# Kernel tuning notes

Measured on AMD Instinct MI355X. Metric: run time of the kernel, lower is better.

## Reference

```python
import jax, jax.numpy as jnp
import numpy as np

NUM_HEADS = 8
CH_PER_HEAD = 32
NUM_GROUPS = 32
EPS = 1e-5
SCALE = CH_PER_HEAD ** (-0.25)


def setup_inputs() -> dict:
    key = jax.random.key(0)
    ks = jax.random.split(key, 6)
    B, C, H, W = 2, 256, 64, 64
    hid = NUM_HEADS * CH_PER_HEAD  # 256
    s = 1.0 / np.sqrt(C)
    return {
        "x": jax.random.normal(ks[0], (B, C, H, W), dtype=jnp.float32),
        "gamma": jnp.ones((C,), jnp.float32),
        "beta": jnp.zeros((C,), jnp.float32),
        "wq": jax.random.normal(ks[1], (hid, C), jnp.float32) * s,
        "bq": jnp.zeros((hid,), jnp.float32),
        "wk": jax.random.normal(ks[2], (hid, C), jnp.float32) * s,
        "bk": jnp.zeros((hid,), jnp.float32),
        "wv": jax.random.normal(ks[3], (hid, C), jnp.float32) * s,
        "bv": jnp.zeros((hid,), jnp.float32),
        "wout": jax.random.normal(ks[4], (C, hid), jnp.float32) * s,
        "bout": jnp.zeros((C,), jnp.float32),
    }


def _group_norm(x, gamma, beta):
    b, c, h, w = x.shape
    xg = x.reshape(b, NUM_GROUPS, c // NUM_GROUPS, h, w)
    mu = jnp.mean(xg, axis=(2, 3, 4), keepdims=True)
    var = jnp.var(xg, axis=(2, 3, 4), keepdims=True)
    xg = (xg - mu) * jax.lax.rsqrt(var + EPS)
    return xg.reshape(b, c, h, w) * gamma[None, :, None, None] + beta[None, :, None, None]


def reference(x, gamma, beta, wq, bq, wk, bk, wv, bv, wout, bout):
    b, c, h, w = x.shape
    n = h * w
    x_n = _group_norm(x, gamma, beta).reshape(b, c, n)  # b c n (self-attention: embedding = x_n)
    # 1x1 convs == pointwise linear over the channel dim
    q = jnp.einsum('oc,bcn->bon', wq, x_n) + bq[None, :, None]
    k = jnp.einsum('oc,bcn->bon', wk, x_n) + bk[None, :, None]
    v = jnp.einsum('oc,bcn->bon', wv, x_n) + bv[None, :, None]
    # split heads: b (h d) n -> b h d n
    d = CH_PER_HEAD
    q = q.reshape(b, NUM_HEADS, d, n)
    k = k.reshape(b, NUM_HEADS, d, n)
    v = v.reshape(b, NUM_HEADS, d, n)
    attn = jax.nn.softmax(jnp.einsum('bhdi,bhdj->bhij', q * SCALE, k * SCALE), axis=-1)
    out = jnp.einsum('bhij,bhdj->bhdi', attn, v).reshape(b, NUM_HEADS * d, n)
    out = jnp.einsum('oc,bcn->bon', wout, out) + bout[None, :, None]
    out = out.reshape(b, -1, h, w)
    return x + out  # shapes match -> residual
```

## Files before the change

### kernel.cpp

```cpp
#include <hip/hip_runtime.h>
#include <hip/hip_bf16.h>
#include <stdint.h>

typedef unsigned short u16;
typedef float f32x4 __attribute__((ext_vector_type(4)));
typedef float f32x16 __attribute__((ext_vector_type(16)));
typedef short bf16x8 __attribute__((ext_vector_type(8)));

#define NSP 4096
#define CDIM 256
#define HID 256
#define NH 8
#define DH 32
#define NG 32
#define CPG 8
#define BATCH 2
#define SPLIT 4
#define GN_EPS 1e-5f
#define QK2_SCALE 0.25503488f

#define MFMA32(A, B, C) __builtin_amdgcn_mfma_f32_32x32x16_bf16(A, B, C, 0, 0, 0)
#define MFMA16(A, B, C) __builtin_amdgcn_mfma_f32_16x16x32_bf16(A, B, C, 0, 0, 0)

__device__ __forceinline__ float bf2f(u16 u) {
    union { uint32_t i; float f; } v; v.i = ((uint32_t)u) << 16; return v.f;
}
__device__ __forceinline__ u16 f2bf(float f) {
    union { float f; uint32_t i; } v; v.f = f;
    uint32_t b = v.i;
    return (u16)((b + 0x7FFFu + ((b >> 16) & 1u)) >> 16);
}

__device__ __forceinline__ void gload16(const u16* g, u16* lds) {
    __builtin_amdgcn_global_load_lds(
        (const __attribute__((address_space(1))) uint32_t*)g,
        (__attribute__((address_space(3))) uint32_t*)lds, 16, 0, 0);
}

__device__ __forceinline__ void pl32swap(uint32_t& a, uint32_t& b) {
    asm("v_permlane32_swap_b32 %0, %1" : "+v"(a), "+v"(b));
}

__global__ void gn_stats(const float* __restrict__ x, float* __restrict__ stats,
                         const float* __restrict__ wq, const float* __restrict__ wk,
                         const float* __restrict__ wv, const float* __restrict__ wout,
                         u16* __restrict__ wcat) {
    int blk = blockIdx.x;
#pragma unroll
    for (int i = 0; i < 16; i++) {
        int idx = blk * 4096 + i * 256 + threadIdx.x;
        const float* src = (idx < 65536) ? wq : (idx < 131072) ? wk : (idx < 196608) ? wv : wout;
        wcat[idx] = f2bf(src[idx & 65535]);
    }
    const float4* base = (const float4*)(x + (size_t)blk * (CPG * NSP));
    float s = 0.f, ss = 0.f;
    for (int i = threadIdx.x; i < (CPG * NSP) / 4; i += 256) {
        float4 v = base[i];
        s  += v.x + v.y + v.z + v.w;
        ss += v.x * v.x + v.y * v.y + v.z * v.z + v.w * v.w;
    }
    for (int m = 1; m < 64; m <<= 1) { s += __shfl_xor(s, m, 64); ss += __shfl_xor(ss, m, 64); }
    __shared__ float ls[4], lss[4];
    int w = threadIdx.x >> 6;
    if ((threadIdx.x & 63) == 0) { ls[w] = s; lss[w] = ss; }
    __syncthreads();
    if (threadIdx.x == 0) {
        float S = ls[0] + ls[1] + ls[2] + ls[3];
        float SS = lss[0] + lss[1] + lss[2] + lss[3];
        float mean = S / (float)(CPG * NSP);
        float var = SS / (float)(CPG * NSP) - mean * mean;
        stats[2 * blk] = mean;
        stats[2 * blk + 1] = rsqrtf(var + GN_EPS);
    }
}

__global__ void gn_apply(const float* __restrict__ x, const float* __restrict__ stats,
                         const float* __restrict__ gamma, const float* __restrict__ beta,
                         u16* __restrict__ xn) {
    __shared__ u16 tile[64][72];
    int n0 = blockIdx.x * 64, c0 = blockIdx.y * 64, b = blockIdx.z;
    int t = threadIdx.x;
    int nl = t & 63, cq = t >> 6;
#pragma unroll
    for (int i = 0; i < 16; i++) {
        int cl = i * 4 + cq;
        int c = c0 + cl;
        int g = c >> 3;
        float mean = stats[2 * (b * NG + g)];
        float rstd = stats[2 * (b * NG + g) + 1];
        float v = x[((size_t)b * CDIM + c) * NSP + n0 + nl];
        v = (v - mean) * rstd * gamma[c] + beta[c];
        tile[cl][nl] = f2bf(v);
    }
    __syncthreads();
    int nr = t >> 2, cc = (t & 3) * 16;
    uint4 o0, o1;
    u16* p0 = (u16*)&o0; u16* p1 = (u16*)&o1;
#pragma unroll
    for (int j = 0; j < 8; j++) { p0[j] = tile[cc + j][nr]; p1[j] = tile[cc + 8 + j][nr]; }
    size_t orow = ((size_t)b * NSP + n0 + nr) * CDIM + c0 + cc;
    *(uint4*)(xn + orow) = o0;
    *(uint4*)(xn + orow + 8) = o1;
}

__global__ __launch_bounds__(256) void gemm_qkv(
    const u16* __restrict__ A, const u16* __restrict__ wcat,
    const float* __restrict__ bq, const float* __restrict__ bk, const float* __restrict__ bv,
    u16* __restrict__ qb, u16* __restrict__ kfb, u16* __restrict__ vfb) {
    __shared__ u16 As[128 * 64];
    __shared__ u16 Bs[128 * 64];
    int bz = blockIdx.z;
    const u16* Ab = A + (size_t)bz * NSP * CDIM;
    int n0 = blockIdx.x * 128, m0 = blockIdx.y * 128;
    int seg = n0 >> 8;
    int t = threadIdx.x, lane = t & 63, w = t >> 6;
    int wr = w >> 1, wc = w & 1;
    f32x4 acc[4][4] = {};

    int srow = w * 8 + (lane >> 3);
    int scol = (lane & 7) * 8;
    const u16* asrc = Ab + (size_t)(m0 + srow) * CDIM + scol;
    const u16* bsrc = wcat + (size_t)(n0 + srow) * CDIM + scol;
    u16* albase = As + w * 512;
    u16* blbase = Bs + w * 512;

    int frow = lane & 15, fcol = (lane >> 4) * 8;

    for (int k0 = 0; k0 < CDIM; k0 += 64) {
        __syncthreads();
#pragma unroll
        for (int ro = 0; ro < 4; ro++) {
            gload16(asrc + (size_t)ro * 32 * CDIM + k0, albase + ro * 2048);
            gload16(bsrc + (size_t)ro * 32 * CDIM + k0, blbase + ro * 2048);
        }
        asm volatile("s_waitcnt vmcnt(0)" ::: "memory");
        __syncthreads();
#pragma unroll
        for (int kk = 0; kk < 2; kk++) {
            bf16x8 af[4], bfv[4];
#pragma unroll
            for (int i = 0; i < 4; i++) {
                af[i]  = *(bf16x8*)&As[(wr * 64 + i * 16 + frow) * 64 + kk * 32 + fcol];
                bfv[i] = *(bf16x8*)&Bs[(wc * 64 + i * 16 + frow) * 64 + kk * 32 + fcol];
            }
#pragma unroll
            for (int i = 0; i < 4; i++)
#pragma unroll
                for (int j = 0; j < 4; j++)
                    acc[i][j] = MFMA16(af[i], bfv[j], acc[i][j]);
        }
    }

    const float* bias = (seg == 0) ? bq : (seg == 1) ? bk : bv;
    int r4 = (lane >> 4) * 4, cx = lane & 15;
#pragma unroll
    for (int i = 0; i < 4; i++) {
        int rbase = m0 + wr * 64 + i * 16 + r4;
#pragma unroll
        for (int j = 0; j < 4; j++) {
            int col = n0 + wc * 64 + j * 16 + cx;
            int cb = col & 255;
            float bb = bias[cb];
            if (seg == 0) {
#pragma unroll
                for (int r = 0; r < 4; r++)
                    qb[(size_t)bz * NSP * HID + (size_t)(rbase + r) * HID + cb] = f2bf(acc[i][j][r] + bb);
            } else if (seg == 1) {
                int h2 = cb >> 5;
                int f = 2 * ((rbase >> 5) & 1) + ((cb >> 4) & 1);
                size_t kt = ((size_t)(bz * NH + h2) * 64 + (rbase >> 6)) * 2048
                          + (size_t)f * 512 + ((rbase & 31) + (((cb >> 3) & 1) << 5)) * 8 + (cb & 7);
#pragma unroll
                for (int r = 0; r < 4; r++)
                    kfb[kt + r * 8] = f2bf((acc[i][j][r] + bb) * QK2_SCALE);
            } else {
                int h2 = cb >> 5, d = cb & 31;
                int jc = (rbase >> 3) & 7;
                size_t vt = ((size_t)(bz * NH + h2) * 64 + (rbase >> 6)) * 2048
                          + (size_t)(jc >> 1) * 512 + (d + ((jc & 1) << 5)) * 8 + (rbase & 7);
                uint2 pkd;
                pkd.x = ((uint32_t)f2bf(acc[i][j][1] + bb) << 16) | f2bf(acc[i][j][0] + bb);
                pkd.y = ((uint32_t)f2bf(acc[i][j][3] + bb) << 16) | f2bf(acc[i][j][2] + bb);
                *(uint2*)(vfb + vt) = pkd;
            }
        }
    }
}

__global__ __launch_bounds__(256) void gemm_out(
    const u16* __restrict__ A,
    const u16* __restrict__ B, long sB,
    const float* __restrict__ bias,
    const float* __restrict__ resid, long sR,
    float* __restrict__ outp, long sO,
    int N) {
    __shared__ u16 As[64][72];
    __shared__ u16 Bs[64][72];
    int bz = blockIdx.z;
    B += (size_t)bz * sB;
    int m0 = blockIdx.y * 64, n0 = blockIdx.x * 64;
    int t = threadIdx.x, lane = t & 63, w = t >> 6;
    int wm = (w >> 1) * 32, wn = (w & 1) * 32;
    f32x4 acc[2][2] = {};

    int sr = t >> 2;
    int sc1 = (t & 3) * 8, sc2 = sc1 + 32;

    uint4 av0 = *(const uint4*)(A + (size_t)(m0 + sr) * CDIM + sc1);
    uint4 av1 = *(const uint4*)(A + (size_t)(m0 + sr) * CDIM + sc2);
    uint4 bv0 = *(const uint4*)(B + (size_t)(n0 + sr) * CDIM + sc1);
    uint4 bv1 = *(const uint4*)(B + (size_t)(n0 + sr) * CDIM + sc2);

    for (int k0 = 0; k0 < CDIM; k0 += 64) {
        __syncthreads();
        *(uint4*)&As[sr][sc1] = av0;
        *(uint4*)&As[sr][sc2] = av1;
        *(uint4*)&Bs[sr][sc1] = bv0;
        *(uint4*)&Bs[sr][sc2] = bv1;
        __syncthreads();
        if (k0 + 64 < CDIM) {
            av0 = *(const uint4*)(A + (size_t)(m0 + sr) * CDIM + k0 + 64 + sc1);
            av1 = *(const uint4*)(A + (size_t)(m0 + sr) * CDIM + k0 + 64 + sc2);
            bv0 = *(const uint4*)(B + (size_t)(n0 + sr) * CDIM + k0 + 64 + sc1);
            bv1 = *(const uint4*)(B + (size_t)(n0 + sr) * CDIM + k0 + 64 + sc2);
        }
#pragma unroll
        for (int ks = 0; ks < 2; ks++) {
            bf16x8 af[2], bfr[2];
#pragma unroll
            for (int i = 0; i < 2; i++) {
                af[i]  = *(bf16x8*)&As[wm + i * 16 + (lane & 15)][ks * 32 + (lane >> 4) * 8];
                bfr[i] = *(bf16x8*)&Bs[wn + i * 16 + (lane & 15)][ks * 32 + (lane >> 4) * 8];
            }
#pragma unroll
            for (int i = 0; i < 2; i++)
#pragma unroll
                for (int j = 0; j < 2; j++)
                    acc[i][j] = MFMA16(af[i], bfr[j], acc[i][j]);
        }
    }

    int r4 = (lane >> 4) * 4, cx = lane & 15;
#pragma unroll
    for (int i = 0; i < 2; i++)
#pragma unroll
        for (int j = 0; j < 2; j++) {
            int rbase = m0 + wm + i * 16 + r4;
            int cbase = n0 + wn + j * 16 + cx;
#pragma unroll
            for (int r = 0; r < 4; r++) {
                int row = rbase + r, col = cbase;
                outp[(size_t)bz * sO + (size_t)row * N + col] =
                    acc[i][j][r] + bias[row] + resid[(size_t)bz * sR + (size_t)row * N + col];
            }
        }
}

__global__ __launch_bounds__(256, 3) void attn_kernel(
    const u16* __restrict__ q, const u16* __restrict__ kfb,
    const u16* __restrict__ vfb, u16* __restrict__ po, float* __restrict__ zz) {
    __shared__ float Ls[4][64];
    int h = blockIdx.y;
    int bz = blockIdx.z;
    int b = bz / SPLIT, sp = bz % SPLIT;
    int kv0 = sp * (NSP / SPLIT);
    int t = threadIdx.x, lane = t & 63, w = t >> 6;
    int ql = lane & 31, hi = lane >> 5;
    int q0 = blockIdx.x * 256 + w * 64;

    const u16* qbp = q + (size_t)b * NSP * HID + (size_t)(q0 + ql) * HID + h * DH + hi * 8;
    bf16x8 qa0 = *(const bf16x8*)(qbp);
    bf16x8 qa1 = *(const bf16x8*)(qbp + 16);
    bf16x8 qb0 = *(const bf16x8*)(qbp + 32 * HID);
    bf16x8 qb1 = *(const bf16x8*)(qbp + 32 * HID + 16);

    size_t tbase = ((size_t)(b * NH + h) * 64 + (kv0 >> 6)) * 2048 + (size_t)lane * 8;
    const u16* kp = kfb + tbase;
    const u16* vp = vfb + tbase;

#define LOADKF(kd, it) { \
    kd[0] = *(const bf16x8*)(kp + (size_t)(it) * 2048);        \
    kd[1] = *(const bf16x8*)(kp + (size_t)(it) * 2048 + 512);  \
    kd[2] = *(const bf16x8*)(kp + (size_t)(it) * 2048 + 1024); \
    kd[3] = *(const bf16x8*)(kp + (size_t)(it) * 2048 + 1536); }
#define LOADVF(vd, it) { \
    vd[0] = *(const bf16x8*)(vp + (size_t)(it) * 2048);        \
    vd[1] = *(const bf16x8*)(vp + (size_t)(it) * 2048 + 512);  \
    vd[2] = *(const bf16x8*)(vp + (size_t)(it) * 2048 + 1024); \
    vd[3] = *(const bf16x8*)(vp + (size_t)(it) * 2048 + 1536); }

    f32x16 kzero = {};
    f32x16 oacc_a = {}, oacc_b = {};
    float la0 = 0.f, la1 = 0.f, lb0 = 0.f, lb1 = 0.f;

    auto softpv = [&](f32x16& st, const bf16x8 (&vf)[4], int tt, f32x16& oacc,
                      float& l0, float& l1) {
        uint32_t pk[8];
#pragma unroll
        for (int j = 0; j < 8; j++) {
            float p0 = __builtin_amdgcn_exp2f(st[2 * j]);
            float p1 = __builtin_amdgcn_exp2f(st[2 * j + 1]);
            float ps = p0 + p1;
            if (j & 1) l1 += ps; else l0 += ps;
            uint32_t dd;
            asm("v_cvt_pk_bf16_f32 %0, %1, %2" : "=v"(dd) : "v"(p0), "v"(p1));
            pk[j] = dd;
        }
#pragma unroll
        for (int c = 0; c < 2; c++) {
            uint32_t a0 = pk[4 * c + 0], b0 = pk[4 * c + 2];
            uint32_t a1 = pk[4 * c + 1], b1 = pk[4 * c + 3];
            pl32swap(a0, b0);
            pl32swap(a1, b1);
            union { uint32_t u[4]; bf16x8 v8; } fr;
            fr.u[0] = a0; fr.u[1] = a1; fr.u[2] = b0; fr.u[3] = b1;
            __builtin_amdgcn_s_setprio(1);
            oacc = MFMA32(fr.v8, vf[2 * tt + c], oacc);
            __builtin_amdgcn_s_setprio(0);
        }
    };

    auto process = [&](const bf16x8 (&kf)[4], const bf16x8 (&vf)[4]) {
#pragma unroll
        for (int tt = 0; tt < 2; tt++) {
            __builtin_amdgcn_s_setprio(1);
            f32x16 st_a = MFMA32(kf[2 * tt], qa0, kzero);
            st_a = MFMA32(kf[2 * tt + 1], qa1, st_a);
            f32x16 st_b = MFMA32(kf[2 * tt], qb0, kzero);
            st_b = MFMA32(kf[2 * tt + 1], qb1, st_b);
            __builtin_amdgcn_s_setprio(0);
            softpv(st_a, vf, tt, oacc_a, la0, la1);
            softpv(st_b, vf, tt, oacc_b, lb0, lb1);
        }
    };

    const int NT = (NSP / SPLIT) / 64;
    bf16x8 k0[4], v0[4], k1[4], v1[4];
    LOADKF(k0, 0); LOADVF(v0, 0);
    LOADKF(k1, 1); LOADVF(v1, 1);
    for (int it = 0; it < NT; it += 2) {
        process(k0, v0);
        int n2 = (it + 2 < NT) ? it + 2 : 0;
        LOADKF(k0, n2); LOADVF(v0, n2);
        process(k1, v1);
        int n3 = (it + 3 < NT) ? it + 3 : 0;
        LOADKF(k1, n3); LOADVF(v1, n3);
    }
#undef LOADKF
#undef LOADVF

    float la = la0 + la1;
    float lb = lb0 + lb1;
    la += __shfl_xor(la, 32);
    lb += __shfl_xor(lb, 32);
    Ls[w][ql] = 1.0f / la;
    Ls[w][32 + ql] = 1.0f / lb;
    if (hi == 0) {
        zz[(((size_t)bz * NH + h) * NSP) + q0 + ql] = __log2f(la);
        zz[(((size_t)bz * NH + h) * NSP) + q0 + 32 + ql] = __log2f(lb);
    }
    u16* pob = po + ((((size_t)bz * NH + h) * NSP) + q0) * DH + ql;
#pragma unroll
    for (int r = 0; r < 16; r++) {
        int qq = (r & 3) + 8 * (r >> 2) + 4 * hi;
        pob[(size_t)qq * DH] = f2bf(oacc_a[r] * Ls[w][qq]);
        pob[(size_t)(32 + qq) * DH] = f2bf(oacc_b[r] * Ls[w][32 + qq]);
    }
}

__global__ __launch_bounds__(256) void combine_kernel(
    const u16* __restrict__ po, const float* __restrict__ zz, u16* __restrict__ ao) {
    int idx = blockIdx.x * 256 + threadIdx.x;
    int c8 = idx & 31;
    int n  = (idx >> 5) & (NSP - 1);
    int b  = idx >> 17;
    int h  = c8 >> 2;
    int dp = (c8 & 3) * 8;

    float z[SPLIT];
    size_t base[SPLIT];
    float M = -3e38f;
#pragma unroll
    for (int s = 0; s < SPLIT; s++) {
        base[s] = ((((size_t)(b * SPLIT + s) * NH + h) * NSP) + n);
        z[s] = zz[base[s]];
        M = fmaxf(M, z[s]);
    }
    float wsum = 0.f, acc[8] = {};
#pragma unroll
    for (int s = 0; s < SPLIT; s++) {
        float ww = __builtin_amdgcn_exp2f(z[s] - M);
        wsum += ww;
        uint4 o = *(const uint4*)(po + base[s] * DH + dp);
        const u16* op = (const u16*)&o;
#pragma unroll
        for (int j = 0; j < 8; j++) acc[j] += bf2f(op[j]) * ww;
    }
    float inv = 1.0f / wsum;
    uint4 r;
    u16* rp = (u16*)&r;
#pragma unroll
    for (int j = 0; j < 8; j++) rp[j] = f2bf(acc[j] * inv);
    *(uint4*)(ao + (((size_t)b * NSP + n) * HID) + h * DH + dp) = r;
}

extern "C" void kernel_launch(void* const* d_in, const int* in_sizes, int n_in,
                              void* d_out, int out_size, void* d_ws, size_t ws_size,
                              hipStream_t stream) {
    const float* x     = (const float*)d_in[0];
    const float* gamma = (const float*)d_in[1];
    const float* beta  = (const float*)d_in[2];
    const float* wq    = (const float*)d_in[3];
    const float* bq    = (const float*)d_in[4];
    const float* wk    = (const float*)d_in[5];
    const float* bk    = (const float*)d_in[6];
    const float* wv    = (const float*)d_in[7];
    const float* bv    = (const float*)d_in[8];
    const float* wout  = (const float*)d_in[9];
    const float* bout  = (const float*)d_in[10];
    float* out = (float*)d_out;

    char* ws = (char*)d_ws;
    float* stats = (float*)ws;
    u16* wq_b = (u16*)(ws + 4096);
    u16* wo_b = wq_b + 3 * 65536;
    u16* xn = wo_b + 65536;
    u16* qb = xn + (size_t)BATCH * NSP * CDIM;
    u16* kfb = qb + (size_t)BATCH * NSP * HID;
    u16* vfb = kfb + (size_t)BATCH * NH * 64 * 2048;
    u16* aob = vfb + (size_t)BATCH * NH * 64 * 2048;
    u16* pob = aob + (size_t)BATCH * NSP * HID;
    float* zzb = (float*)(pob + (size_t)SPLIT * BATCH * NH * NSP * DH);

    const long sQ = (long)NSP * HID;
    const long sOut = (long)CDIM * NSP;

    gn_stats<<<BATCH * NG, 256, 0, stream>>>(x, stats, wq, wk, wv, wout, wq_b);
    gn_apply<<<dim3(NSP / 64, CDIM / 64, BATCH), 256, 0, stream>>>(x, stats, gamma, beta, xn);

    gemm_qkv<<<dim3(768 / 128, NSP / 128, BATCH), 256, 0, stream>>>(
        xn, wq_b, bq, bk, bv, qb, kfb, vfb);

    attn_kernel<<<dim3(NSP / 256, NH, BATCH * SPLIT), 256, 0, stream>>>(qb, kfb, vfb, pob, zzb);
    combine_kernel<<<(BATCH * NSP * HID / 8) / 256, 256, 0, stream>>>(pob, zzb, aob);

    gemm_out<<<dim3(NSP / 64, CDIM / 64, BATCH), 256, 0, stream>>>(
        wo_b, aob, sQ, bout, x, sOut, out, sOut, NSP);
}
```

Before: 91.64 us.

## Split GroupNorm stats across more blocks and stage QKV epilogue through LDS

GroupNorm statistics are now computed by 512 blocks producing partial sums, and gn_apply reduces the eight partials per group itself. This raises parallelism over the earlier 64-block stats pass. The QKV GEMM epilogue now writes its bf16 results into a padded shared-memory tile and then emits 16-byte coalesced stores into the Q, K-fragment and V-fragment layouts, replacing scattered 2-byte and 8-byte stores. The cost is extra LDS traffic, added barriers, and a small redundant partial reduction in every gn_apply block.

```diff
diff --git a/kernel.cpp b/kernel.cpp
--- a/kernel.cpp
+++ b/kernel.cpp
@@ -41,53 +41,67 @@
     asm("v_permlane32_swap_b32 %0, %1" : "+v"(a), "+v"(b));
 }
 
-__global__ void gn_stats(const float* __restrict__ x, float* __restrict__ stats,
-                         const float* __restrict__ wq, const float* __restrict__ wk,
-                         const float* __restrict__ wv, const float* __restrict__ wout,
-                         u16* __restrict__ wcat) {
+__global__ __launch_bounds__(256) void stats_partial(
+    const float* __restrict__ x, float* __restrict__ partials,
+    const float* __restrict__ wq, const float* __restrict__ wk,
+    const float* __restrict__ wv, const float* __restrict__ wout,
+    u16* __restrict__ wcat) {
     int blk = blockIdx.x;
-#pragma unroll
-    for (int i = 0; i < 16; i++) {
-        int idx = blk * 4096 + i * 256 + threadIdx.x;
+    int t = threadIdx.x;
+#pragma unroll
+    for (int i = 0; i < 2; i++) {
+        int idx = blk * 512 + i * 256 + t;
         const float* src = (idx < 65536) ? wq : (idx < 131072) ? wk : (idx < 196608) ? wv : wout;
         wcat[idx] = f2bf(src[idx & 65535]);
     }
-    const float4* base = (const float4*)(x + (size_t)blk * (CPG * NSP));
+    int bg = blk >> 3, sl = blk & 7;
+    const float4* base = (const float4*)(x + (size_t)bg * (CPG * NSP) + sl * 4096);
     float s = 0.f, ss = 0.f;
-    for (int i = threadIdx.x; i < (CPG * NSP) / 4; i += 256) {
-        float4 v = base[i];
+#pragma unroll
+    for (int i = 0; i < 4; i++) {
+        float4 v = base[t + i * 256];
         s  += v.x + v.y + v.z + v.w;
         ss += v.x * v.x + v.y * v.y + v.z * v.z + v.w * v.w;
     }
     for (int m = 1; m < 64; m <<= 1) { s += __shfl_xor(s, m, 64); ss += __shfl_xor(ss, m, 64); }
     __shared__ float ls[4], lss[4];
-    int w = threadIdx.x >> 6;
-    if ((threadIdx.x & 63) == 0) { ls[w] = s; lss[w] = ss; }
+    int w = t >> 6;
+    if ((t & 63) == 0) { ls[w] = s; lss[w] = ss; }
     __syncthreads();
-    if (threadIdx.x == 0) {
-        float S = ls[0] + ls[1] + ls[2] + ls[3];
-        float SS = lss[0] + lss[1] + lss[2] + lss[3];
-        float mean = S / (float)(CPG * NSP);
-        float var = SS / (float)(CPG * NSP) - mean * mean;
-        stats[2 * blk] = mean;
-        stats[2 * blk + 1] = rsqrtf(var + GN_EPS);
-    }
-}
-
-__global__ void gn_apply(const float* __restrict__ x, const float* __restrict__ stats,
+    if (t == 0) {
+        partials[bg * 16 + sl * 2]     = ls[0] + ls[1] + ls[2] + ls[3];
+        partials[bg * 16 + sl * 2 + 1] = lss[0] + lss[1] + lss[2] + lss[3];
+    }
+}
+
+__global__ void gn_apply(const float* __restrict__ x, const float* __restrict__ partials,
                          const float* __restrict__ gamma, const float* __restrict__ beta,
                          u16* __restrict__ xn) {
     __shared__ u16 tile[64][72];
+    __shared__ float mr[8][2];
     int n0 = blockIdx.x * 64, c0 = blockIdx.y * 64, b = blockIdx.z;
     int t = threadIdx.x;
+    if (t < 8) {
+        int bg = b * NG + (c0 >> 3) + t;
+        float s = 0.f, ss = 0.f;
+#pragma unroll
+        for (int sl = 0; sl < 8; sl++) {
+            s  += partials[bg * 16 + sl * 2];
+            ss += partials[bg * 16 + sl * 2 + 1];
+        }
+        float mean = s * (1.0f / 32768.0f);
+        float var = ss * (1.0f / 32768.0f) - mean * mean;
+        mr[t][0] = mean;
+        mr[t][1] = rsqrtf(var + GN_EPS);
+    }
+    __syncthreads();
     int nl = t & 63, cq = t >> 6;
 #pragma unroll
     for (int i = 0; i < 16; i++) {
         int cl = i * 4 + cq;
         int c = c0 + cl;
-        int g = c >> 3;
-        float mean = stats[2 * (b * NG + g)];
-        float rstd = stats[2 * (b * NG + g) + 1];
+        float mean = mr[cl >> 3][0];
+        float rstd = mr[cl >> 3][1];
         float v = x[((size_t)b * CDIM + c) * NSP + n0 + nl];
         v = (v - mean) * rstd * gamma[c] + beta[c];
         tile[cl][nl] = f2bf(v);
@@ -107,8 +121,9 @@
     const u16* __restrict__ A, const u16* __restrict__ wcat,
     const float* __restrict__ bq, const float* __restrict__ bk, const float* __restrict__ bv,
     u16* __restrict__ qb, u16* __restrict__ kfb, u16* __restrict__ vfb) {
-    __shared__ u16 As[128 * 64];
-    __shared__ u16 Bs[128 * 64];
+    __shared__ u16 SMEM[128 * 136];
+    u16* As = SMEM;
+    u16* Bs = SMEM + 8192;
     int bz = blockIdx.z;
     const u16* Ab = A + (size_t)bz * NSP * CDIM;
     int n0 = blockIdx.x * 128, m0 = blockIdx.y * 128;
@@ -153,36 +168,74 @@
 
     const float* bias = (seg == 0) ? bq : (seg == 1) ? bk : bv;
     int r4 = (lane >> 4) * 4, cx = lane & 15;
-#pragma unroll
-    for (int i = 0; i < 4; i++) {
-        int rbase = m0 + wr * 64 + i * 16 + r4;
-#pragma unroll
-        for (int j = 0; j < 4; j++) {
-            int col = n0 + wc * 64 + j * 16 + cx;
-            int cb = col & 255;
-            float bb = bias[cb];
-            if (seg == 0) {
-#pragma unroll
-                for (int r = 0; r < 4; r++)
-                    qb[(size_t)bz * NSP * HID + (size_t)(rbase + r) * HID + cb] = f2bf(acc[i][j][r] + bb);
-            } else if (seg == 1) {
-                int h2 = cb >> 5;
-                int f = 2 * ((rbase >> 5) & 1) + ((cb >> 4) & 1);
-                size_t kt = ((size_t)(bz * NH + h2) * 64 + (rbase >> 6)) * 2048
-                          + (size_t)f * 512 + ((rbase & 31) + (((cb >> 3) & 1) << 5)) * 8 + (cb & 7);
-#pragma unroll
-                for (int r = 0; r < 4; r++)
-                    kfb[kt + r * 8] = f2bf((acc[i][j][r] + bb) * QK2_SCALE);
-            } else {
-                int h2 = cb >> 5, d = cb & 31;
-                int jc = (rbase >> 3) & 7;
-                size_t vt = ((size_t)(bz * NH + h2) * 64 + (rbase >> 6)) * 2048
-                          + (size_t)(jc >> 1) * 512 + (d + ((jc & 1) << 5)) * 8 + (rbase & 7);
-                uint2 pkd;
-                pkd.x = ((uint32_t)f2bf(acc[i][j][1] + bb) << 16) | f2bf(acc[i][j][0] + bb);
-                pkd.y = ((uint32_t)f2bf(acc[i][j][3] + bb) << 16) | f2bf(acc[i][j][2] + bb);
-                *(uint2*)(vfb + vt) = pkd;
-            }
+    const int STR = 136;
+    __syncthreads();
+
+    if (seg <= 1) {
+#pragma unroll
+        for (int i = 0; i < 4; i++) {
+            int row_l = wr * 64 + i * 16 + r4;
+#pragma unroll
+            for (int j = 0; j < 4; j++) {
+                int col_l = wc * 64 + j * 16 + cx;
+                float bb = bias[(n0 & 255) + col_l];
+#pragma unroll
+                for (int r = 0; r < 4; r++) {
+                    float vv = acc[i][j][r] + bb;
+                    if (seg == 1) vv *= QK2_SCALE;
+                    SMEM[(row_l + r) * STR + col_l] = f2bf(vv);
+                }
+            }
+        }
+        __syncthreads();
+        if (seg == 0) {
+#pragma unroll
+            for (int i = 0; i < 8; i++) {
+                int c = i * 256 + t;
+                int row = c >> 4, o = c & 15;
+                uint4 v = *(uint4*)&SMEM[row * STR + o * 8];
+                *(uint4*)(qb + (size_t)bz * NSP * HID + (size_t)(m0 + row) * HID + (n0 & 255) + o * 8) = v;
+            }
+        } else {
+#pragma unroll
+            for (int i = 0; i < 8; i++) {
+                int c = i * 256 + t;
+                int rl = c & 127, o = c >> 7;
+                int colg = (n0 & 255) + o * 8;
+                int h2 = colg >> 5;
+                int rg = m0 + rl;
+                int f = 2 * ((rg >> 5) & 1) + ((colg >> 4) & 1);
+                size_t off = ((size_t)(bz * NH + h2) * 64 + (rg >> 6)) * 2048 + (size_t)f * 512
+                           + (size_t)(rg & 31) * 8 + (size_t)((colg >> 3) & 1) * 256;
+                *(uint4*)(kfb + off) = *(uint4*)&SMEM[rl * STR + o * 8];
+            }
+        }
+    } else {
+#pragma unroll
+        for (int i = 0; i < 4; i++) {
+            int row_l = wr * 64 + i * 16 + r4;
+#pragma unroll
+            for (int j = 0; j < 4; j++) {
+                int col_l = wc * 64 + j * 16 + cx;
+                float bb = bias[(n0 & 255) + col_l];
+                uint2 pk2;
+                pk2.x = ((uint32_t)f2bf(acc[i][j][1] + bb) << 16) | f2bf(acc[i][j][0] + bb);
+                pk2.y = ((uint32_t)f2bf(acc[i][j][3] + bb) << 16) | f2bf(acc[i][j][2] + bb);
+                *(uint2*)&SMEM[col_l * STR + row_l] = pk2;
+            }
+        }
+        __syncthreads();
+#pragma unroll
+        for (int i = 0; i < 8; i++) {
+            int c = i * 256 + t;
+            int dl = c & 127, jl = c >> 7;
+            int colg = (n0 & 255) + dl;
+            int h2 = colg >> 5, d = colg & 31;
+            int ng = m0 + jl * 8;
+            int jc = (ng >> 3) & 7;
+            size_t off = ((size_t)(bz * NH + h2) * 64 + (ng >> 6)) * 2048 + (size_t)(jc >> 1) * 512
+                       + (size_t)(d + (jc & 1) * 32) * 8;
+            *(uint4*)(vfb + off) = *(uint4*)&SMEM[dl * STR + jl * 8];
         }
     }
 }
@@ -421,7 +474,7 @@
     float* out = (float*)d_out;
 
     char* ws = (char*)d_ws;
-    float* stats = (float*)ws;
+    float* partials = (float*)ws;
     u16* wq_b = (u16*)(ws + 4096);
     u16* wo_b = wq_b + 3 * 65536;
     u16* xn = wo_b + 65536;
@@ -435,8 +488,8 @@
     const long sQ = (long)NSP * HID;
     const long sOut = (long)CDIM * NSP;
 
-    gn_stats<<<BATCH * NG, 256, 0, stream>>>(x, stats, wq, wk, wv, wout, wq_b);
-    gn_apply<<<dim3(NSP / 64, CDIM / 64, BATCH), 256, 0, stream>>>(x, stats, gamma, beta, xn);
+    stats_partial<<<512, 256, 0, stream>>>(x, partials, wq, wk, wv, wout, wq_b);
+    gn_apply<<<dim3(NSP / 64, CDIM / 64, BATCH), 256, 0, stream>>>(x, partials, gamma, beta, xn);
 
     gemm_qkv<<<dim3(768 / 128, NSP / 128, BATCH), 256, 0, stream>>>(
         xn, wq_b, bq, bk, bv, qb, kfb, vfb);
```

Measured after the change: 83.59 us. -8.8%, faster.
